# Optimization experiments

Measured on AMD Instinct MI355X. Metric: run time of the kernel, lower is better.

## Reference

```python
import jax, jax.numpy as jnp
import numpy as np
import math

HEAD_SIZE = 64

def setup_inputs() -> dict:
    key = jax.random.key(0)
    k0, k1, k2, k3 = jax.random.split(key, 4)
    B, T, E, H = 4, 4096, 1024, HEAD_SIZE
    return {
        "x": jax.random.normal(k0, (B, T, E), dtype=jnp.float32),
        "Wq": jax.random.normal(k1, (E, H), dtype=jnp.float32) * (1.0 / math.sqrt(E)),
        "Wk": jax.random.normal(k2, (E, H), dtype=jnp.float32) * (1.0 / math.sqrt(E)),
        "Wv": jax.random.normal(k3, (E, H), dtype=jnp.float32) * (1.0 / math.sqrt(E)),
    }

def reference(x, Wq, Wk, Wv):
    # Single-head attention; faithful to source: softmax FIRST, then divide by sqrt(head_size)
    T = x.shape[-2]
    q = x @ Wq  # [B,T,H]
    k = x @ Wk
    v = x @ Wv
    scores = jnp.einsum('bth,bsh->bts', q, k)  # [B,T,T]
    # 'encoder' mask in this repo = lower-triangular (causal)
    causal = jnp.tril(jnp.ones((T, T), dtype=bool))
    scores = jnp.where(causal, scores, -jnp.inf)
    attn = jax.nn.softmax(scores, axis=-1) / jnp.sqrt(jnp.float32(q.shape[-1]))
    return jnp.einsum('bts,bsh->bth', attn, v)
```

## Files before the change

### kernel.cpp

```cpp
#include <hip/hip_runtime.h>
#include <math.h>

#define BB 4
#define TT 4096
#define EE 1024
#define HH 64

typedef __attribute__((ext_vector_type(8))) short bf16x8;
typedef __attribute__((ext_vector_type(4))) float f32x4;
typedef __attribute__((ext_vector_type(16))) float f32x16;

#define MFMA16(a, b, c) __builtin_amdgcn_mfma_f32_16x16x32_bf16(a, b, c, 0, 0, 0)
#define MFMA32(a, b, c) __builtin_amdgcn_mfma_f32_32x32x16_bf16(a, b, c, 0, 0, 0)

__device__ __forceinline__ unsigned short f2bf_rne(float f) {
    unsigned u = __float_as_uint(f);
    unsigned r = u + 0x7fffu + ((u >> 16) & 1u);
    return (unsigned short)(r >> 16);
}
__device__ __forceinline__ float bf2f(unsigned short h) {
    return __uint_as_float(((unsigned)h) << 16);
}

__device__ __forceinline__ void async_copy16(const void* g, void* l) {
    __builtin_amdgcn_global_load_lds(
        (const __attribute__((address_space(1))) void*)g,
        (__attribute__((address_space(3))) void*)l, 16, 0, 0);
}
template<int N>
__device__ __forceinline__ void wait_vm() {
    __builtin_amdgcn_s_waitcnt(0x0f70 | (N & 15) | ((N >> 4) << 14));
}

__global__ __launch_bounds__(256) void wprep_kernel(
    const float* __restrict__ Wq, const float* __restrict__ Wk,
    const float* __restrict__ Wv,
    unsigned short* __restrict__ wt_hi, unsigned short* __restrict__ wt_lo)
{
    __shared__ float ts[64][65];
    const int which = blockIdx.x >> 4;
    const int e0 = (blockIdx.x & 15) * 64;
    const float* W = (which == 0) ? Wq : ((which == 1) ? Wk : Wv);
    const int t = threadIdx.x;
    const int h = t & 63;
    #pragma unroll
    for (int p = 0; p < 16; p++) {
        const int er = (t >> 6) + p * 4;
        ts[er][h] = W[(size_t)(e0 + er) * 64 + h];
    }
    __syncthreads();
    const int ew = t & 63;
    #pragma unroll
    for (int p = 0; p < 16; p++) {
        const int hh = (t >> 6) + p * 4;
        const float f = ts[ew][hh];
        const unsigned short hb = f2bf_rne(f);
        const unsigned short lb = f2bf_rne(f - bf2f(hb));
        const size_t o = (size_t)(which * 64 + hh) * 1024 + e0 + ew;
        wt_hi[o] = hb;
        wt_lo[o] = lb;
    }
}

__global__ __launch_bounds__(512) void proj_kernel(
    const float* __restrict__ x,
    const unsigned short* __restrict__ wt_hi, const unsigned short* __restrict__ wt_lo,
    unsigned short* __restrict__ qhi, unsigned short* __restrict__ qlo,
    unsigned short* __restrict__ khi, unsigned short* __restrict__ klo,
    unsigned short* __restrict__ vt)
{
    __shared__ __align__(16) unsigned char smem[98304];
    const int tid = threadIdx.x;
    const int w = tid >> 6, lane = tid & 63;
    const int l31 = lane & 31, kh = lane >> 5;
    const int tg = w & 1, eh = (w >> 1) & 1, hh = w >> 2;
    const int row0 = (int)blockIdx.x * 64;
    const int tok = row0 + tg * 32 + l31;

    f32x16 acc[3];
    #pragma unroll
    for (int mt = 0; mt < 3; mt++)
        #pragma unroll
        for (int r = 0; r < 16; r++) acc[mt][r] = 0.f;

    const float* xr = x + (size_t)tok * EE + eh * 512 + kh * 8;

    const int r_l = lane >> 3, sl = lane & 7;
    const int cg = sl ^ r_l;
    const unsigned short* mat = (cg < 4) ? wt_hi : wt_lo;
    const int ce = (cg & 3) * 8;

    auto dma_step = [&](int e0, unsigned char* dstbase) {
        #pragma unroll
        for (int ii = 0; ii < 6; ii++) {
            const int i = w * 6 + ii;
            const int ehc = i / 24;
            const int within = i % 24;
            const int row = within * 8 + r_l;
            const unsigned short* src = mat + (size_t)row * EE + ehc * 512 + e0 + ce;
            async_copy16(src, dstbase + ehc * 24576 + within * 1024);
        }
    };

    const int r7 = lane & 7;
    const int sh0 = ((0 * 2 + kh) ^ r7) * 16;
    const int sl0 = ((4 + 0 * 2 + kh) ^ r7) * 16;
    const int sh1 = ((1 * 2 + kh) ^ r7) * 16;
    const int sl1 = ((4 + 1 * 2 + kh) ^ r7) * 16;

    dma_step(0, smem);
    float4 fc0 = *(const float4*)(xr + 0);
    float4 fc1 = *(const float4*)(xr + 4);
    float4 fc2 = *(const float4*)(xr + 16);
    float4 fc3 = *(const float4*)(xr + 20);
    float4 fn0, fn1, fn2, fn3;

    for (int s = 0; s < 16; s++) {
        wait_vm<0>();
        __builtin_amdgcn_s_barrier();
        if (s < 15) {
            const int e1 = (s + 1) * 32;
            dma_step(e1, smem + ((s + 1) & 1) * 49152);
            fn0 = *(const float4*)(xr + e1);
            fn1 = *(const float4*)(xr + e1 + 4);
            fn2 = *(const float4*)(xr + e1 + 16);
            fn3 = *(const float4*)(xr + e1 + 20);
        }

        float f0[8] = {fc0.x, fc0.y, fc0.z, fc0.w, fc1.x, fc1.y, fc1.z, fc1.w};
        float f1[8] = {fc2.x, fc2.y, fc2.z, fc2.w, fc3.x, fc3.y, fc3.z, fc3.w};
        bf16x8 bh0, bl0, bh1, bl1;
        #pragma unroll
        for (int jj = 0; jj < 8; jj++) {
            unsigned short hb;
            hb = f2bf_rne(f0[jj]); bh0[jj] = (short)hb;
            bl0[jj] = (short)f2bf_rne(f0[jj] - bf2f(hb));
            hb = f2bf_rne(f1[jj]); bh1[jj] = (short)hb;
            bl1[jj] = (short)f2bf_rne(f1[jj] - bf2f(hb));
        }

        const unsigned char* Wbase = smem + (s & 1) * 49152 + eh * 24576;
        #pragma unroll
        for (int mt = 0; mt < 3; mt++) {
            const unsigned char* rb = Wbase + (hh * 96 + mt * 32 + l31) * 128;
            bf16x8 Ah0 = *(const bf16x8*)(rb + sh0);
            bf16x8 Al0 = *(const bf16x8*)(rb + sl0);
            bf16x8 Ah1 = *(const bf16x8*)(rb + sh1);
            bf16x8 Al1 = *(const bf16x8*)(rb + sl1);
            acc[mt] = MFMA32(Ah0, bh0, acc[mt]);
            acc[mt] = MFMA32(Ah0, bl0, acc[mt]);
            acc[mt] = MFMA32(Al0, bh0, acc[mt]);
            acc[mt] = MFMA32(Ah1, bh1, acc[mt]);
            acc[mt] = MFMA32(Ah1, bl1, acc[mt]);
            acc[mt] = MFMA32(Al1, bh1, acc[mt]);
        }
        fc0 = fn0; fc1 = fn1; fc2 = fn2; fc3 = fn3;
    }

    __syncthreads();
    float* Red = (float*)smem;
    if (eh == 1) {
        #pragma unroll
        for (int mt = 0; mt < 3; mt++)
            #pragma unroll
            for (int r = 0; r < 16; r++) {
                const int H = hh * 96 + mt * 32 + (r & 3) + 8 * (r >> 2) + 4 * kh;
                Red[(size_t)(tg * 192 + H) * 33 + l31] = acc[mt][r];
            }
    }
    __syncthreads();
    if (eh == 0) {
        #pragma unroll
        for (int mt = 0; mt < 3; mt++)
            #pragma unroll
            for (int r = 0; r < 16; r++) {
                const int H = hh * 96 + mt * 32 + (r & 3) + 8 * (r >> 2) + 4 * kh;
                acc[mt][r] += Red[(size_t)(tg * 192 + H) * 33 + l31];
            }
        const int bb = tok >> 12, tloc = tok & 4095;
        #pragma unroll
        for (int mt = 0; mt < 3; mt++) {
            #pragma unroll
            for (int gq = 0; gq < 4; gq++) {
                const int Hc = hh * 96 + mt * 32 + gq * 8;
                const int H0 = Hc + kh * 4;
                float fv[4] = {acc[mt][gq * 4 + 0], acc[mt][gq * 4 + 1],
                               acc[mt][gq * 4 + 2], acc[mt][gq * 4 + 3]};
                if (Hc < 64) {
                    ushort4 hi4, lo4; unsigned short hb;
                    hb = f2bf_rne(fv[0]); hi4.x = hb; lo4.x = f2bf_rne(fv[0] - bf2f(hb));
                    hb = f2bf_rne(fv[1]); hi4.y = hb; lo4.y = f2bf_rne(fv[1] - bf2f(hb));
                    hb = f2bf_rne(fv[2]); hi4.z = hb; lo4.z = f2bf_rne(fv[2] - bf2f(hb));
                    hb = f2bf_rne(fv[3]); hi4.w = hb; lo4.w = f2bf_rne(fv[3] - bf2f(hb));
                    const size_t o = (size_t)tok * 64 + H0;
                    *(ushort4*)(qhi + o) = hi4; *(ushort4*)(qlo + o) = lo4;
                } else if (Hc < 128) {
                    ushort4 hi4, lo4; unsigned short hb;
                    hb = f2bf_rne(fv[0]); hi4.x = hb; lo4.x = f2bf_rne(fv[0] - bf2f(hb));
                    hb = f2bf_rne(fv[1]); hi4.y = hb; lo4.y = f2bf_rne(fv[1] - bf2f(hb));
                    hb = f2bf_rne(fv[2]); hi4.z = hb; lo4.z = f2bf_rne(fv[2] - bf2f(hb));
                    hb = f2bf_rne(fv[3]); hi4.w = hb; lo4.w = f2bf_rne(fv[3] - bf2f(hb));
                    const size_t o = (size_t)tok * 64 + (H0 - 64);
                    *(ushort4*)(khi + o) = hi4; *(ushort4*)(klo + o) = lo4;
                } else {
                    #pragma unroll
                    for (int r = 0; r < 4; r++)
                        vt[((size_t)(bb * 64 + (H0 - 128) + r) << 12) + tloc] =
                            f2bf_rne(fv[r]);
                }
            }
        }
    }
}

__global__ __launch_bounds__(512) void flash_kernel(
    const unsigned short* __restrict__ qhi, const unsigned short* __restrict__ qlo,
    const unsigned short* __restrict__ khi, const unsigned short* __restrict__ klo,
    const unsigned short* __restrict__ vt, float* __restrict__ out)
{
    __shared__ __align__(16) unsigned char smem[151552];
    const int tid = threadIdx.x;
    const int w = tid >> 6, lane = tid & 63;
    const int quad = lane >> 4, li = lane & 15;
    const int bx = (int)blockIdx.x;
    const int b = (int)blockIdx.y;
    const float SM = 20.0f;

    const unsigned short* kb_hi = khi + ((size_t)b << 18);
    const unsigned short* kb_lo = klo + ((size_t)b << 18);
    const unsigned short* vtb   = vt  + ((size_t)b << 18) + (size_t)li * 4096 + quad * 8;

    unsigned char* kbase = smem + w * 16384;
    unsigned short* PsA = (unsigned short*)(smem + 131072 + w * 2560);
    unsigned short* PsB = PsA + 640;
    float* Op = (float*)smem;
    float* Ml = (float*)(smem + 67584);

    const int r_l4 = lane >> 4, s16 = lane & 15;
    const int slh0 = ((quad)      ^ li) * 8;
    const int slh1 = ((4 + quad)  ^ li) * 8;
    const int sll0 = ((8 + quad)  ^ li) * 8;
    const int sll1 = ((12 + quad) ^ li) * 8;

    auto dma_tile = [&](int k0, unsigned char* dst) {
        #pragma unroll
        for (int i = 0; i < 8; i++) {
            const int row = i * 4 + r_l4;
            const int c = s16 ^ (row & 15);
            const unsigned short* src = (c < 8)
                ? kb_hi + (size_t)(k0 + row) * 64 + c * 8
                : kb_lo + (size_t)(k0 + row) * 64 + (c - 8) * 8;
            async_copy16(src, dst + i * 1024);
        }
    };

    #pragma unroll 1
    for (int phase = 0; phase < 2; phase++) {
        const int g = phase ? (127 - bx) : bx;
        const int q0 = g * 32;
        const int n_kt = g + 1;
        const int tok0 = q0 + li, tok1 = tok0 + 16;

        const size_t qo0 = ((size_t)(b << 12) + tok0) * 64 + quad * 8;
        const size_t qo1 = qo0 + 16 * 64;
        const bf16x8 QhA0 = *(const bf16x8*)(qhi + qo0);
        const bf16x8 QhA1 = *(const bf16x8*)(qhi + qo0 + 32);
        const bf16x8 QlA0 = *(const bf16x8*)(qlo + qo0);
        const bf16x8 QlA1 = *(const bf16x8*)(qlo + qo0 + 32);
        const bf16x8 QhB0 = *(const bf16x8*)(qhi + qo1);
        const bf16x8 QhB1 = *(const bf16x8*)(qhi + qo1 + 32);
        const bf16x8 QlB0 = *(const bf16x8*)(qlo + qo1);
        const bf16x8 QlB1 = *(const bf16x8*)(qlo + qo1 + 32);

        f32x4 accA[4], accB[4];
        #pragma unroll
        for (int mt = 0; mt < 4; mt++) {
            accA[mt] = (f32x4){0.f, 0.f, 0.f, 0.f};
            accB[mt] = (f32x4){0.f, 0.f, 0.f, 0.f};
        }
        float lA = 0.f, lB = 0.f;

        bf16x8 Vc[4], Vn[4];
        int bufp = 0;
        if (w < n_kt) {
            dma_tile(w * 32, kbase);
            #pragma unroll
            for (int hf = 0; hf < 4; hf++)
                Vc[hf] = *(const bf16x8*)(vtb + (size_t)hf * 65536 + w * 32);
        }

        for (int kt = w; kt < n_kt; kt += 8) {
            const int k0 = kt * 32;

            if (kt + 8 < n_kt) {
                dma_tile((kt + 8) * 32, kbase + (bufp ^ 1) * 8192);
                #pragma unroll
                for (int hf = 0; hf < 4; hf++)
                    Vn[hf] = *(const bf16x8*)(vtb + (size_t)hf * 65536 + (kt + 8) * 32);
                wait_vm<12>();
            } else {
                wait_vm<0>();
            }
            const unsigned short* Kw = (const unsigned short*)(kbase + bufp * 8192);

            f32x4 sA[2], sB[2];
            #pragma unroll
            for (int jf = 0; jf < 2; jf++) {
                const unsigned short* rb = Kw + (jf * 16 + li) * 128;
                bf16x8 Kh0 = *(const bf16x8*)(rb + slh0);
                bf16x8 Kh1 = *(const bf16x8*)(rb + slh1);
                bf16x8 Kl0 = *(const bf16x8*)(rb + sll0);
                bf16x8 Kl1 = *(const bf16x8*)(rb + sll1);
                f32x4 a = (f32x4){0.f, 0.f, 0.f, 0.f};
                a = MFMA16(Kh0, QhA0, a);
                a = MFMA16(Kh1, QhA1, a);
                a = MFMA16(Kh0, QlA0, a);
                a = MFMA16(Kh1, QlA1, a);
                a = MFMA16(Kl0, QhA0, a);
                a = MFMA16(Kl1, QhA1, a);
                sA[jf] = a;
                f32x4 c2 = (f32x4){0.f, 0.f, 0.f, 0.f};
                c2 = MFMA16(Kh0, QhB0, c2);
                c2 = MFMA16(Kh1, QhB1, c2);
                c2 = MFMA16(Kh0, QlB0, c2);
                c2 = MFMA16(Kh1, QlB1, c2);
                c2 = MFMA16(Kl0, QhB0, c2);
                c2 = MFMA16(Kl1, QhB1, c2);
                sB[jf] = c2;
            }

            if (kt == n_kt - 1) {
                #pragma unroll
                for (int jf = 0; jf < 2; jf++)
                    #pragma unroll
                    for (int r = 0; r < 4; r++) {
                        const int j = k0 + jf * 16 + quad * 4 + r;
                        if (j > tok0) sA[jf][r] = -1e30f;
                        if (j > tok1) sB[jf][r] = -1e30f;
                    }
            }

            #pragma unroll
            for (int jf = 0; jf < 2; jf++)
                #pragma unroll
                for (int r = 0; r < 4; r++) {
                    sA[jf][r] = __expf(sA[jf][r] - SM); lA += sA[jf][r];
                    sB[jf][r] = __expf(sB[jf][r] - SM); lB += sB[jf][r];
                }

            #pragma unroll
            for (int jf = 0; jf < 2; jf++) {
                ushort4 pa, pb;
                pa.x = f2bf_rne(sA[jf][0]); pa.y = f2bf_rne(sA[jf][1]);
                pa.z = f2bf_rne(sA[jf][2]); pa.w = f2bf_rne(sA[jf][3]);
                pb.x = f2bf_rne(sB[jf][0]); pb.y = f2bf_rne(sB[jf][1]);
                pb.z = f2bf_rne(sB[jf][2]); pb.w = f2bf_rne(sB[jf][3]);
                *(ushort4*)&PsA[li * 40 + jf * 16 + quad * 4] = pa;
                *(ushort4*)&PsB[li * 40 + jf * 16 + quad * 4] = pb;
            }
            const bf16x8 PA = *(const bf16x8*)&PsA[li * 40 + quad * 8];
            const bf16x8 PB = *(const bf16x8*)&PsB[li * 40 + quad * 8];

            #pragma unroll
            for (int hf = 0; hf < 4; hf++) {
                accA[hf] = MFMA16(Vc[hf], PA, accA[hf]);
                accB[hf] = MFMA16(Vc[hf], PB, accB[hf]);
            }
            #pragma unroll
            for (int hf = 0; hf < 4; hf++) Vc[hf] = Vn[hf];
            bufp ^= 1;
        }

        lA += __shfl_xor(lA, 16); lA += __shfl_xor(lA, 32);
        lB += __shfl_xor(lB, 16); lB += __shfl_xor(lB, 32);

        __syncthreads();
        #pragma unroll
        for (int mt = 0; mt < 4; mt++)
            #pragma unroll
            for (int r = 0; r < 4; r++) {
                Op[(size_t)w * 2112 + (mt * 16 + quad * 4 + r) * 33 + li]      = accA[mt][r];
                Op[(size_t)w * 2112 + (mt * 16 + quad * 4 + r) * 33 + li + 16] = accB[mt][r];
            }
        if (quad == 0) {
            Ml[w * 32 + li]      = lA;
            Ml[w * 32 + 16 + li] = lB;
        }
        __syncthreads();

        const int i  = tid >> 4;
        const int hc = (tid & 15) * 4;
        float l = 0.f;
        #pragma unroll
        for (int ww = 0; ww < 8; ww++) l += Ml[ww * 32 + i];
        const float inv = 1.0f / (l * 8.0f);
        float4 o = {0.f, 0.f, 0.f, 0.f};
        #pragma unroll
        for (int ww = 0; ww < 8; ww++) {
            const float* base = Op + (size_t)ww * 2112;
            o.x += base[(hc + 0) * 33 + i];
            o.y += base[(hc + 1) * 33 + i];
            o.z += base[(hc + 2) * 33 + i];
            o.w += base[(hc + 3) * 33 + i];
        }
        o.x *= inv; o.y *= inv; o.z *= inv; o.w *= inv;
        *(float4*)(out + ((size_t)(b << 12) + q0 + i) * 64 + hc) = o;
        __syncthreads();
    }
}

extern "C" void kernel_launch(void* const* d_in, const int* in_sizes, int n_in,
                              void* d_out, int out_size, void* d_ws, size_t ws_size,
                              hipStream_t stream)
{
    const float* x  = (const float*)d_in[0];
    const float* Wq = (const float*)d_in[1];
    const float* Wk = (const float*)d_in[2];
    const float* Wv = (const float*)d_in[3];
    float* out = (float*)d_out;

    const size_t n_tok = (size_t)BB * TT * HH;
    unsigned short* qhi = (unsigned short*)d_ws;
    unsigned short* qlo = qhi + n_tok;
    unsigned short* khi = qlo + n_tok;
    unsigned short* klo = khi + n_tok;
    unsigned short* vt  = klo + n_tok;
    unsigned short* wt_hi = vt + n_tok;
    unsigned short* wt_lo = wt_hi + 192 * 1024;

    wprep_kernel<<<48, 256, 0, stream>>>(Wq, Wk, Wv, wt_hi, wt_lo);
    proj_kernel<<<(BB * TT) / 64, 512, 0, stream>>>(x, wt_hi, wt_lo,
                                                    qhi, qlo, khi, klo, vt);
    flash_kernel<<<dim3(64, BB), 512, 0, stream>>>(qhi, qlo, khi, klo, vt, out);
}
```

Measured before the change: 162.9 us.

## Restructure projection kernel: 32-token blocks, six waves each owning a head slice

The projection kernel now handles 32 tokens per block with 6 waves. Each wave owns one 32-wide slice of the 192 QKV output columns and loops over the full embedding dimension, so no split-K is needed. This removes the cross-wave shared-memory reduction and its extra barriers, halves LDS use and doubles the grid size. In exchange each block streams all of W per 32 tokens, doubling weight traffic per token, and every wave reloads the same x rows.

After: 208.0 us. 27.7% more time.

```diff
diff --git a/kernel.cpp b/kernel.cpp
--- a/kernel.cpp
+++ b/kernel.cpp
@@ -62,73 +62,67 @@
     }
 }
 
-__global__ __launch_bounds__(512) void proj_kernel(
+__global__ __launch_bounds__(384) void proj_kernel(
     const float* __restrict__ x,
     const unsigned short* __restrict__ wt_hi, const unsigned short* __restrict__ wt_lo,
     unsigned short* __restrict__ qhi, unsigned short* __restrict__ qlo,
     unsigned short* __restrict__ khi, unsigned short* __restrict__ klo,
     unsigned short* __restrict__ vt)
 {
-    __shared__ __align__(16) unsigned char smem[98304];
+    __shared__ __align__(16) unsigned char smem[49152];
     const int tid = threadIdx.x;
     const int w = tid >> 6, lane = tid & 63;
     const int l31 = lane & 31, kh = lane >> 5;
-    const int tg = w & 1, eh = (w >> 1) & 1, hh = w >> 2;
-    const int row0 = (int)blockIdx.x * 64;
-    const int tok = row0 + tg * 32 + l31;
-
-    f32x16 acc[3];
+    const int row0 = (int)blockIdx.x * 32;
+    const int tok = row0 + l31;
+
+    f32x16 acc;
     #pragma unroll
-    for (int mt = 0; mt < 3; mt++)
-        #pragma unroll
-        for (int r = 0; r < 16; r++) acc[mt][r] = 0.f;
-
-    const float* xr = x + (size_t)tok * EE + eh * 512 + kh * 8;
+    for (int r = 0; r < 16; r++) acc[r] = 0.f;
+
+    const float* xr = x + (size_t)tok * EE + kh * 8;
 
     const int r_l = lane >> 3, sl = lane & 7;
     const int cg = sl ^ r_l;
     const unsigned short* mat = (cg < 4) ? wt_hi : wt_lo;
     const int ce = (cg & 3) * 8;
 
-    auto dma_step = [&](int e0, unsigned char* dstbase) {
-        #pragma unroll
-        for (int ii = 0; ii < 6; ii++) {
-            const int i = w * 6 + ii;
-            const int ehc = i / 24;
-            const int within = i % 24;
-            const int row = within * 8 + r_l;
-            const unsigned short* src = mat + (size_t)row * EE + ehc * 512 + e0 + ce;
-            async_copy16(src, dstbase + ehc * 24576 + within * 1024);
+    auto dma_step = [&](int e0, unsigned char* dst) {
+        #pragma unroll
+        for (int ii = 0; ii < 4; ii++) {
+            const int i = w * 4 + ii;
+            const int row = i * 8 + r_l;
+            async_copy16(mat + (size_t)row * EE + e0 + ce, dst + i * 1024);
         }
     };
 
     const int r7 = lane & 7;
-    const int sh0 = ((0 * 2 + kh) ^ r7) * 16;
-    const int sl0 = ((4 + 0 * 2 + kh) ^ r7) * 16;
-    const int sh1 = ((1 * 2 + kh) ^ r7) * 16;
-    const int sl1 = ((4 + 1 * 2 + kh) ^ r7) * 16;
+    const int sh0 = ((0 + kh) ^ r7) * 16;
+    const int sl0 = ((4 + kh) ^ r7) * 16;
+    const int sh1 = ((2 + kh) ^ r7) * 16;
+    const int sl1 = ((6 + kh) ^ r7) * 16;
 
     dma_step(0, smem);
-    float4 fc0 = *(const float4*)(xr + 0);
-    float4 fc1 = *(const float4*)(xr + 4);
-    float4 fc2 = *(const float4*)(xr + 16);
-    float4 fc3 = *(const float4*)(xr + 20);
-    float4 fn0, fn1, fn2, fn3;
-
-    for (int s = 0; s < 16; s++) {
+    float4 c0 = *(const float4*)(xr + 0);
+    float4 c1 = *(const float4*)(xr + 4);
+    float4 c2 = *(const float4*)(xr + 16);
+    float4 c3 = *(const float4*)(xr + 20);
+    float4 n0, n1, n2, n3;
+
+    for (int s = 0; s < 32; s++) {
         wait_vm<0>();
         __builtin_amdgcn_s_barrier();
-        if (s < 15) {
+        if (s < 31) {
             const int e1 = (s + 1) * 32;
-            dma_step(e1, smem + ((s + 1) & 1) * 49152);
-            fn0 = *(const float4*)(xr + e1);
-            fn1 = *(const float4*)(xr + e1 + 4);
-            fn2 = *(const float4*)(xr + e1 + 16);
-            fn3 = *(const float4*)(xr + e1 + 20);
-        }
-
-        float f0[8] = {fc0.x, fc0.y, fc0.z, fc0.w, fc1.x, fc1.y, fc1.z, fc1.w};
-        float f1[8] = {fc2.x, fc2.y, fc2.z, fc2.w, fc3.x, fc3.y, fc3.z, fc3.w};
+            dma_step(e1, smem + ((s + 1) & 1) * 24576);
+            n0 = *(const float4*)(xr + e1);
+            n1 = *(const float4*)(xr + e1 + 4);
+            n2 = *(const float4*)(xr + e1 + 16);
+            n3 = *(const float4*)(xr + e1 + 20);
+        }
+
+        float f0[8] = {c0.x, c0.y, c0.z, c0.w, c1.x, c1.y, c1.z, c1.w};
+        float f1[8] = {c2.x, c2.y, c2.z, c2.w, c3.x, c3.y, c3.z, c3.w};
         bf16x8 bh0, bl0, bh1, bl1;
         #pragma unroll
         for (int jj = 0; jj < 8; jj++) {
@@ -139,76 +133,44 @@
             bl1[jj] = (short)f2bf_rne(f1[jj] - bf2f(hb));
         }
 
-        const unsigned char* Wbase = smem + (s & 1) * 49152 + eh * 24576;
-        #pragma unroll
-        for (int mt = 0; mt < 3; mt++) {
-            const unsigned char* rb = Wbase + (hh * 96 + mt * 32 + l31) * 128;
-            bf16x8 Ah0 = *(const bf16x8*)(rb + sh0);
-            bf16x8 Al0 = *(const bf16x8*)(rb + sl0);
-            bf16x8 Ah1 = *(const bf16x8*)(rb + sh1);
-            bf16x8 Al1 = *(const bf16x8*)(rb + sl1);
-            acc[mt] = MFMA32(Ah0, bh0, acc[mt]);
-            acc[mt] = MFMA32(Ah0, bl0, acc[mt]);
-            acc[mt] = MFMA32(Al0, bh0, acc[mt]);
-            acc[mt] = MFMA32(Ah1, bh1, acc[mt]);
-            acc[mt] = MFMA32(Ah1, bl1, acc[mt]);
-            acc[mt] = MFMA32(Al1, bh1, acc[mt]);
-        }
-        fc0 = fn0; fc1 = fn1; fc2 = fn2; fc3 = fn3;
-    }
-
-    __syncthreads();
-    float* Red = (float*)smem;
-    if (eh == 1) {
-        #pragma unroll
-        for (int mt = 0; mt < 3; mt++)
-            #pragma unroll
-            for (int r = 0; r < 16; r++) {
-                const int H = hh * 96 + mt * 32 + (r & 3) + 8 * (r >> 2) + 4 * kh;
-                Red[(size_t)(tg * 192 + H) * 33 + l31] = acc[mt][r];
-            }
-    }
-    __syncthreads();
-    if (eh == 0) {
-        #pragma unroll
-        for (int mt = 0; mt < 3; mt++)
-            #pragma unroll
-            for (int r = 0; r < 16; r++) {
-                const int H = hh * 96 + mt * 32 + (r & 3) + 8 * (r >> 2) + 4 * kh;
-                acc[mt][r] += Red[(size_t)(tg * 192 + H) * 33 + l31];
-            }
-        const int bb = tok >> 12, tloc = tok & 4095;
-        #pragma unroll
-        for (int mt = 0; mt < 3; mt++) {
-            #pragma unroll
-            for (int gq = 0; gq < 4; gq++) {
-                const int Hc = hh * 96 + mt * 32 + gq * 8;
-                const int H0 = Hc + kh * 4;
-                float fv[4] = {acc[mt][gq * 4 + 0], acc[mt][gq * 4 + 1],
-                               acc[mt][gq * 4 + 2], acc[mt][gq * 4 + 3]};
-                if (Hc < 64) {
-                    ushort4 hi4, lo4; unsigned short hb;
-                    hb = f2bf_rne(fv[0]); hi4.x = hb; lo4.x = f2bf_rne(fv[0] - bf2f(hb));
-                    hb = f2bf_rne(fv[1]); hi4.y = hb; lo4.y = f2bf_rne(fv[1] - bf2f(hb));
-                    hb = f2bf_rne(fv[2]); hi4.z = hb; lo4.z = f2bf_rne(fv[2] - bf2f(hb));
-                    hb = f2bf_rne(fv[3]); hi4.w = hb; lo4.w = f2bf_rne(fv[3] - bf2f(hb));
-                    const size_t o = (size_t)tok * 64 + H0;
-                    *(ushort4*)(qhi + o) = hi4; *(ushort4*)(qlo + o) = lo4;
-                } else if (Hc < 128) {
-                    ushort4 hi4, lo4; unsigned short hb;
-                    hb = f2bf_rne(fv[0]); hi4.x = hb; lo4.x = f2bf_rne(fv[0] - bf2f(hb));
-                    hb = f2bf_rne(fv[1]); hi4.y = hb; lo4.y = f2bf_rne(fv[1] - bf2f(hb));
-                    hb = f2bf_rne(fv[2]); hi4.z = hb; lo4.z = f2bf_rne(fv[2] - bf2f(hb));
-                    hb = f2bf_rne(fv[3]); hi4.w = hb; lo4.w = f2bf_rne(fv[3] - bf2f(hb));
-                    const size_t o = (size_t)tok * 64 + (H0 - 64);
-                    *(ushort4*)(khi + o) = hi4; *(ushort4*)(klo + o) = lo4;
-                } else {
-                    #pragma unroll
-                    for (int r = 0; r < 4; r++)
-                        vt[((size_t)(bb * 64 + (H0 - 128) + r) << 12) + tloc] =
-                            f2bf_rne(fv[r]);
-                }
-            }
+        const unsigned char* rb =
+            smem + (s & 1) * 24576 + (w * 32 + l31) * 128;
+        bf16x8 Ah0 = *(const bf16x8*)(rb + sh0);
+        bf16x8 Al0 = *(const bf16x8*)(rb + sl0);
+        bf16x8 Ah1 = *(const bf16x8*)(rb + sh1);
+        bf16x8 Al1 = *(const bf16x8*)(rb + sl1);
+        acc = MFMA32(Ah0, bh0, acc);
+        acc = MFMA32(Ah0, bl0, acc);
+        acc = MFMA32(Al0, bh0, acc);
+        acc = MFMA32(Ah1, bh1, acc);
+        acc = MFMA32(Ah1, bl1, acc);
+        acc = MFMA32(Al1, bh1, acc);
+        c0 = n0; c1 = n1; c2 = n2; c3 = n3;
+    }
+
+    const int bb = tok >> 12, tloc = tok & 4095;
+    if (w < 4) {
+        unsigned short* hi_p = (w < 2) ? qhi : khi;
+        unsigned short* lo_p = (w < 2) ? qlo : klo;
+        const int hbase = (w & 1) * 32;
+        #pragma unroll
+        for (int g = 0; g < 4; g++) {
+            const int h = hbase + g * 8 + kh * 4;
+            ushort4 hi4, lo4; unsigned short hb; float f;
+            f = acc[g * 4 + 0]; hb = f2bf_rne(f); hi4.x = hb; lo4.x = f2bf_rne(f - bf2f(hb));
+            f = acc[g * 4 + 1]; hb = f2bf_rne(f); hi4.y = hb; lo4.y = f2bf_rne(f - bf2f(hb));
+            f = acc[g * 4 + 2]; hb = f2bf_rne(f); hi4.z = hb; lo4.z = f2bf_rne(f - bf2f(hb));
+            f = acc[g * 4 + 3]; hb = f2bf_rne(f); hi4.w = hb; lo4.w = f2bf_rne(f - bf2f(hb));
+            const size_t o = (size_t)tok * 64 + h;
+            *(ushort4*)(hi_p + o) = hi4;
+            *(ushort4*)(lo_p + o) = lo4;
+        }
+    } else {
+        const int hbase = (w - 4) * 32;
+        #pragma unroll
+        for (int r = 0; r < 16; r++) {
+            const int H = hbase + (r & 3) + 8 * (r >> 2) + 4 * kh;
+            vt[((size_t)(bb * 64 + H) << 12) + tloc] = f2bf_rne(acc[r]);
         }
     }
 }
@@ -429,7 +391,7 @@
     unsigned short* wt_lo = wt_hi + 192 * 1024;
 
     wprep_kernel<<<48, 256, 0, stream>>>(Wq, Wk, Wv, wt_hi, wt_lo);
-    proj_kernel<<<(BB * TT) / 64, 512, 0, stream>>>(x, wt_hi, wt_lo,
+    proj_kernel<<<(BB * TT) / 32, 384, 0, stream>>>(x, wt_hi, wt_lo,
                                                     qhi, qlo, khi, klo, vt);
     flash_kernel<<<dim3(64, BB), 512, 0, stream>>>(qhi, qlo, khi, klo, vt, out);
 }
```
